# Performance work log

Hardware: AMD Instinct MI355X
Metric: run time of the kernel (lower is better)

## Reference

```python
import jax, jax.numpy as jnp
import numpy as np

N_NODES = 100000
N_EDGES = 1600000
D_IN = 128
D_HID = 128
LATENT = 64
N_GRAPHS = 512


def setup_inputs() -> dict:
    key = jax.random.key(0)
    ks = jax.random.split(key, 10)
    x = jax.random.normal(ks[0], (N_NODES, D_IN), dtype=jnp.float32)
    edge_index = jax.random.randint(ks[1], (2, N_EDGES), 0, N_NODES, dtype=jnp.int64)
    batch = jnp.sort(jax.random.randint(ks[2], (N_NODES,), 0, N_GRAPHS, dtype=jnp.int64))
    def lin(k, fan_in, fan_out):
        return jax.random.normal(k, (fan_in, fan_out), dtype=jnp.float32) / np.sqrt(fan_in)
    W1 = lin(ks[3], D_IN, D_HID); b1 = jnp.zeros((D_HID,), jnp.float32)
    W2 = lin(ks[4], D_HID, D_HID); b2 = jnp.zeros((D_HID,), jnp.float32)
    W3 = lin(ks[5], D_HID, 2 * LATENT); b3 = jnp.zeros((2 * LATENT,), jnp.float32)
    return {"x": x, "edge_index": edge_index, "batch": batch,
            "W1": W1, "b1": b1, "W2": W2, "b2": b2, "W3": W3, "b3": b3}


def _gcn_norm(edge_index, n_nodes):
    # PyG GCNConv default: add self-loops, symmetric normalization
    loop = jnp.arange(n_nodes, dtype=edge_index.dtype)
    src = jnp.concatenate([edge_index[0], loop])
    dst = jnp.concatenate([edge_index[1], loop])
    deg = jax.ops.segment_sum(jnp.ones_like(dst, dtype=jnp.float32), dst,
                              num_segments=n_nodes)
    dinv = jnp.where(deg > 0, jax.lax.rsqrt(deg), 0.0)
    norm = dinv[src] * dinv[dst]  # [E + N]
    return src, dst, norm


def _gcn_conv(x, W, b, src, dst, norm, n_nodes):
    h = x @ W                               # [N, d_out]
    msg = h[src] * norm[:, None]            # gather + scale, [E+N, d_out]
    agg = jax.ops.segment_sum(msg, dst, num_segments=n_nodes)
    return agg + b


def reference(x, edge_index, batch, W1, b1, W2, b2, W3, b3):
    n = x.shape[0]
    src, dst, norm = _gcn_norm(edge_index, n)
    h = jax.nn.relu(_gcn_conv(x, W1, b1, src, dst, norm, n))
    h = jax.nn.relu(_gcn_conv(h, W2, b2, src, dst, norm, n))
    h = _gcn_conv(h, W3, b3, src, dst, norm, n)
    # scatter_mean over batch ids -> [num_graphs, 2*latent]
    cnt = jax.ops.segment_sum(jnp.ones((n,), jnp.float32), batch,
                              num_segments=N_GRAPHS)
    summed = jax.ops.segment_sum(h, batch, num_segments=N_GRAPHS)
    return summed / jnp.maximum(cnt, 1.0)[:, None]
```

## Files before the change

### kernel.cpp

```cpp
#include <hip/hip_runtime.h>
#include <stdint.h>

typedef unsigned short u16;
typedef unsigned int   u32;

#define N_NODES  100000
#define N_EDGES  1600000
#define DFEAT    128
#define N_GRAPHS 512

#define NBKT   391
#define NBLK_E 782
#define LBUF   8192

typedef float f32x4 __attribute__((ext_vector_type(4)));
typedef short s16x8 __attribute__((ext_vector_type(8)));

__device__ __forceinline__ float bflo(u32 u) { return __uint_as_float(u << 16); }
__device__ __forceinline__ float bfhi(u32 u) { return __uint_as_float(u & 0xffff0000u); }
__device__ __forceinline__ u16 f2bf(float f) {
  u32 u = __float_as_uint(f);
  return (u16)((u + 0x7fffu + ((u >> 16) & 1u)) >> 16);
}
__device__ __forceinline__ u32 pack2(float f0, float f1) {
  return (u32)f2bf(f0) | ((u32)f2bf(f1) << 16);
}

__global__ void detect_k(const int* __restrict__ ei, int* __restrict__ flag) {
  int t = threadIdx.x;
  int v = ei[2 * t + 1];
  unsigned long long m = __ballot(v != 0);
  if (t == 0) *flag = (m == 0ull) ? 1 : 0;
}

__device__ __forceinline__ int ld_src(const int* ei, int m, int e) {
  return m ? ei[2 * e] : ei[e];
}
__device__ __forceinline__ int ld_dst(const int* ei, int m, int e) {
  return m ? ei[2 * (N_EDGES + e)] : ei[N_EDGES + e];
}


__global__ __launch_bounds__(256) void histA_k(const int* __restrict__ ei,
                                               const int* __restrict__ flag,
                                               int* __restrict__ ghist) {
  __shared__ int hist[NBKT];
  int t = threadIdx.x, b = blockIdx.x;
  for (int i = t; i < NBKT; i += 256) hist[i] = 0;
  __syncthreads();
  int m = *flag;
  int e0 = b * 2048;
#pragma unroll
  for (int p = 0; p < 8; p++) {
    int e = e0 + p * 256 + t;
    if (e < N_EDGES) atomicAdd(&hist[ld_dst(ei, m, e) >> 8], 1);
  }
  __syncthreads();
  for (int i = t; i < NBKT; i += 256) ghist[b * NBKT + i] = hist[i];
}

__global__ __launch_bounds__(256) void scanB1_k(int* __restrict__ ghist,
                                                int* __restrict__ gtot) {
  __shared__ int a[1024];
  __shared__ int ts[256];
  int t = threadIdx.x, k = blockIdx.x;
  for (int i = t; i < 1024; i += 256) a[i] = (i < NBLK_E) ? ghist[i * NBKT + k] : 0;
  __syncthreads();
  int b4 = t * 4;
  int x0 = a[b4], x1 = a[b4 + 1], x2 = a[b4 + 2], x3 = a[b4 + 3];
  int tot = x0 + x1 + x2 + x3;
  ts[t] = tot;
  for (int off = 1; off < 256; off <<= 1) {
    __syncthreads(); int add = (t >= off) ? ts[t - off] : 0;
    __syncthreads(); ts[t] += add;
  }
  __syncthreads();
  int excl = ts[t] - tot;
  a[b4] = excl; a[b4 + 1] = excl + x0; a[b4 + 2] = excl + x0 + x1; a[b4 + 3] = excl + x0 + x1 + x2;
  __syncthreads();
  for (int i = t; i < NBLK_E; i += 256) ghist[i * NBKT + k] = a[i];
  if (t == 255) gtot[k] = ts[255];
}

__global__ __launch_bounds__(512) void scanB2_k(const int* __restrict__ gtot,
                                                int* __restrict__ bbase) {
  __shared__ int tmp[512];
  int t = threadIdx.x;
  int v = (t < NBKT) ? gtot[t] : 0;
  tmp[t] = v;
  for (int off = 1; off < 512; off <<= 1) {
    __syncthreads(); int add = (t >= off) ? tmp[t - off] : 0;
    __syncthreads(); tmp[t] += add;
  }
  __syncthreads();
  if (t < NBKT) bbase[t] = tmp[t] - v;
  if (t == 0) bbase[NBKT] = N_EDGES;
}

__global__ __launch_bounds__(256) void scatterC_k(const int* __restrict__ ei,
                                                  const int* __restrict__ flag,
                                                  const int* __restrict__ obase,
                                                  const int* __restrict__ bbase,
                                                  u32* __restrict__ colpk) {
  __shared__ int cur[NBKT];
  int t = threadIdx.x, b = blockIdx.x;
  for (int i = t; i < NBKT; i += 256) cur[i] = bbase[i] + obase[b * NBKT + i];
  __syncthreads();
  int m = *flag;
  int e0 = b * 2048;
#pragma unroll
  for (int p = 0; p < 8; p++) {
    int e = e0 + p * 256 + t;
    if (e < N_EDGES) {
      int d = ld_dst(ei, m, e);
      int s = ld_src(ei, m, e);
      int pos = atomicAdd(&cur[d >> 8], 1);
      colpk[pos] = (u32)s | ((u32)(d & 255) << 24);
    }
  }
}

__global__ __launch_bounds__(256) void fillD_k(const int* __restrict__ bbase,
                                               const u32* __restrict__ colpk,
                                               int* __restrict__ colarr,
                                               int* __restrict__ rowptr,
                                               float* __restrict__ dinv) {
  __shared__ int hist[256];
  __shared__ int cur[256];
  __shared__ int lbuf[LBUF];
  int t = threadIdx.x, b = blockIdx.x;
  int base = bbase[b], end = bbase[b + 1], cnt = end - base;
  hist[t] = 0;
  __syncthreads();
  for (int i = t; i < cnt; i += 256) atomicAdd(&hist[colpk[base + i] >> 24], 1);
  __syncthreads();
  int c = hist[t];
  cur[t] = c;
  for (int off = 1; off < 256; off <<= 1) {
    __syncthreads(); int add = (t >= off) ? cur[t - off] : 0;
    __syncthreads(); cur[t] += add;
  }
  __syncthreads();
  int excl = cur[t] - c;
  int node = b * 256 + t;
  if (node < N_NODES) {
    rowptr[node] = base + excl;
    dinv[node] = rsqrtf((float)(c + 1));
  }
  if (b == NBKT - 1 && t == 0) rowptr[N_NODES] = N_EDGES;
  __syncthreads();
  cur[t] = excl;
  __syncthreads();
  for (int i = t; i < cnt; i += 256) {
    u32 v = colpk[base + i];
    int slot = atomicAdd(&cur[v >> 24], 1);
    if (slot < LBUF) lbuf[slot] = (int)(v & 0x00FFFFFFu);
  }
  __syncthreads();
  for (int i = t; i < cnt; i += 256) colarr[base + i] = lbuf[i];
}

__global__ void cvt_x_k(const float* __restrict__ X, u32* __restrict__ XB) {
  int i = blockIdx.x * 256 + threadIdx.x;
  float2 v = ((const float2*)X)[i];
  XB[i] = pack2(v.x, v.y);
}

__global__ void cvt_w_k(const float* __restrict__ W1, const float* __restrict__ W2,
                        const float* __restrict__ W3, u16* __restrict__ T1,
                        u16* __restrict__ T2, u16* __restrict__ T3) {
  const float* W = (blockIdx.x == 0) ? W1 : (blockIdx.x == 1) ? W2 : W3;
  u16* T         = (blockIdx.x == 0) ? T1 : (blockIdx.x == 1) ? T2 : T3;
  for (int i = threadIdx.x; i < DFEAT * DFEAT; i += 256) {
    int n = i >> 7, k = i & 127;
    T[i] = f2bf(W[k * DFEAT + n]);
  }
}

#define LP 136

__global__ __launch_bounds__(256, 1) void gemm_scale_k(const u16* __restrict__ X,
                                                       const u16* __restrict__ Wt,
                                                       const float* __restrict__ dinv,
                                                       u16* __restrict__ Y, int nrows) {
  __shared__ u16 sX[64 * LP];
  __shared__ u16 sW[128 * LP];
  int tid = threadIdx.x;
  int r0 = blockIdx.x * 64;

  for (int c = tid; c < 2048; c += 256) {
    int row = c >> 4, off = (c & 15) * 8;
    *(uint4*)(&sW[row * LP + off]) = *(const uint4*)(Wt + row * DFEAT + off);
  }
  for (int c = tid; c < 1024; c += 256) {
    int row = c >> 4, off = (c & 15) * 8;
    int grow = r0 + row;
    uint4 v;
    if (grow < nrows) v = *(const uint4*)(X + (size_t)grow * DFEAT + off);
    else              v = make_uint4(0, 0, 0, 0);
    *(uint4*)(&sX[row * LP + off]) = v;
  }
  __syncthreads();

  int wave = tid >> 6, lane = tid & 63;
  int q = lane >> 4, r = lane & 15;
  int wr0 = wave * 16;

  f32x4 acc[8];
#pragma unroll
  for (int i = 0; i < 8; i++) acc[i] = (f32x4){0.f, 0.f, 0.f, 0.f};

#pragma unroll
  for (int kk = 0; kk < 4; kk++) {
    int k0 = kk * 32;
    s16x8 a = *(const s16x8*)(&sX[(wr0 + r) * LP + k0 + q * 8]);
#pragma unroll
    for (int nt = 0; nt < 8; nt++) {
      s16x8 b = *(const s16x8*)(&sW[(nt * 16 + r) * LP + k0 + q * 8]);
      acc[nt] = __builtin_amdgcn_mfma_f32_16x16x32_bf16(a, b, acc[nt], 0, 0, 0);
    }
  }

#pragma unroll
  for (int i = 0; i < 4; i++) {
    int grow = r0 + wr0 + q * 4 + i;
    if (grow < nrows) {
      float dv = dinv[grow];
#pragma unroll
      for (int nt = 0; nt < 8; nt++) {
        Y[(size_t)grow * DFEAT + nt * 16 + r] = f2bf(acc[nt][i] * dv);
      }
    }
  }
}

struct Acc8 {
  float a0, a1, a2, a3, a4, a5, a6, a7;
  __device__ __forceinline__ void add(uint4 v) {
    a0 += bflo(v.x); a1 += bfhi(v.x); a2 += bflo(v.y); a3 += bfhi(v.y);
    a4 += bflo(v.z); a5 += bfhi(v.z); a6 += bflo(v.w); a7 += bfhi(v.w);
  }
};

__global__ __launch_bounds__(256) void agg_k(const u32* __restrict__ HS,
                                             const float* __restrict__ dinv,
                                             const int* __restrict__ rowptr,
                                             const int* __restrict__ colidx,
                                             const float* __restrict__ bias,
                                             u32* __restrict__ OUT, int do_relu) {
  int t = threadIdx.x;
  int node = blockIdx.x * 16 + (t >> 4);
  int fp = t & 15;

  int s = rowptr[node], e = rowptr[node + 1];

  Acc8 A;
  uint4 v = *(const uint4*)(HS + (size_t)node * 64 + fp * 4);
  A.a0 = bflo(v.x); A.a1 = bfhi(v.x); A.a2 = bflo(v.y); A.a3 = bfhi(v.y);
  A.a4 = bflo(v.z); A.a5 = bfhi(v.z); A.a6 = bflo(v.w); A.a7 = bfhi(v.w);

  int j = s;
  for (; j + 4 <= e; j += 4) {
    int i0 = colidx[j], i1 = colidx[j + 1], i2 = colidx[j + 2], i3 = colidx[j + 3];
    uint4 w0 = *(const uint4*)(HS + (size_t)i0 * 64 + fp * 4);
    uint4 w1 = *(const uint4*)(HS + (size_t)i1 * 64 + fp * 4);
    uint4 w2 = *(const uint4*)(HS + (size_t)i2 * 64 + fp * 4);
    uint4 w3 = *(const uint4*)(HS + (size_t)i3 * 64 + fp * 4);
    A.add(w0); A.add(w1); A.add(w2); A.add(w3);
  }
  for (; j < e; j++) {
    int i0 = colidx[j];
    uint4 w0 = *(const uint4*)(HS + (size_t)i0 * 64 + fp * 4);
    A.add(w0);
  }

  float dv = dinv[node];
  float4 b0 = *(const float4*)(bias + fp * 8);
  float4 b1 = *(const float4*)(bias + fp * 8 + 4);
  float r0 = A.a0 * dv + b0.x, r1 = A.a1 * dv + b0.y;
  float r2 = A.a2 * dv + b0.z, r3 = A.a3 * dv + b0.w;
  float r4 = A.a4 * dv + b1.x, r5 = A.a5 * dv + b1.y;
  float r6 = A.a6 * dv + b1.z, r7 = A.a7 * dv + b1.w;
  if (do_relu) {
    r0 = fmaxf(r0, 0.f); r1 = fmaxf(r1, 0.f); r2 = fmaxf(r2, 0.f); r3 = fmaxf(r3, 0.f);
    r4 = fmaxf(r4, 0.f); r5 = fmaxf(r5, 0.f); r6 = fmaxf(r6, 0.f); r7 = fmaxf(r7, 0.f);
  }
  uint4 o;
  o.x = pack2(r0, r1); o.y = pack2(r2, r3); o.z = pack2(r4, r5); o.w = pack2(r6, r7);
  *(uint4*)(OUT + (size_t)node * 64 + fp * 4) = o;
}

__device__ __forceinline__ int lower_bound_i(const int* a, int n, int key, int shift) {
  int lo = 0, hi = n;
  while (lo < hi) {
    int mid = (lo + hi) >> 1;
    if (a[mid << shift] < key) lo = mid + 1; else hi = mid;
  }
  return lo;
}

__global__ __launch_bounds__(256) void pool_k(const u32* __restrict__ H,
                                              const int* __restrict__ batch,
                                              const int* __restrict__ flag,
                                              float* __restrict__ OUT) {
  int g = blockIdx.x;
  int m = *flag;
  int lo = lower_bound_i(batch, N_NODES, g, m);
  int hi = lower_bound_i(batch, N_NODES, g + 1, m);
  int cnt = hi - lo;
  int d2 = threadIdx.x & 63;
  int half = threadIdx.x >> 6;
  float a0 = 0.f, a1 = 0.f;
  for (int row = lo + half; row < hi; row += 4) {
    u32 v = H[(size_t)row * 64 + d2];
    a0 += bflo(v); a1 += bfhi(v);
  }
  __shared__ float red0[256], red1[256];
  red0[threadIdx.x] = a0; red1[threadIdx.x] = a1;
  __syncthreads();
  if (threadIdx.x < 64) {
    float s0 = red0[d2] + red0[d2 + 64] + red0[d2 + 128] + red0[d2 + 192];
    float s1 = red1[d2] + red1[d2 + 64] + red1[d2 + 128] + red1[d2 + 192];
    float inv = 1.0f / fmaxf((float)cnt, 1.0f);
    OUT[g * DFEAT + 2 * d2]     = s0 * inv;
    OUT[g * DFEAT + 2 * d2 + 1] = s1 * inv;
  }
}


extern "C" void kernel_launch(void* const* d_in, const int* in_sizes, int n_in,
                              void* d_out, int out_size, void* d_ws, size_t ws_size,
                              hipStream_t stream) {
  const float* x   = (const float*)d_in[0];
  const int* ei    = (const int*)d_in[1];
  const int* batch = (const int*)d_in[2];
  const float* W1  = (const float*)d_in[3];
  const float* b1  = (const float*)d_in[4];
  const float* W2  = (const float*)d_in[5];
  const float* b2  = (const float*)d_in[6];
  const float* W3  = (const float*)d_in[7];
  const float* b3  = (const float*)d_in[8];
  float* out = (float*)d_out;

  char* p = (char*)d_ws;
  size_t off = 0;
  auto carve = [&](size_t bytes) -> void* {
    void* q = p + off;
    off = (off + bytes + 255) & ~(size_t)255;
    return q;
  };
  int*   flag   = (int*)carve(256);
  int*   ghist  = (int*)carve((size_t)NBLK_E * NBKT * 4);
  int*   gtot   = (int*)carve(NBKT * 4);
  int*   bbase  = (int*)carve((NBKT + 1) * 4);
  int*   rowptr = (int*)carve((N_NODES + 1) * 4);
  float* dinv   = (float*)carve(N_NODES * 4);
  u32*   colpk  = (u32*)carve((size_t)N_EDGES * 4);
  int*   colarr = (int*)carve((size_t)N_EDGES * 4);
  u16*   Wt1    = (u16*)carve(DFEAT * DFEAT * 2);
  u16*   Wt2    = (u16*)carve(DFEAT * DFEAT * 2);
  u16*   Wt3    = (u16*)carve(DFEAT * DFEAT * 2);
  u32*   xb     = (u32*)carve((size_t)N_NODES * 64 * 4);
  u32*   bufA   = (u32*)carve((size_t)N_NODES * 64 * 4);
  u32*   bufB   = (u32*)carve((size_t)N_NODES * 64 * 4);
  (void)ws_size;

  detect_k<<<1, 64, 0, stream>>>(ei, flag);
  histA_k<<<NBLK_E, 256, 0, stream>>>(ei, flag, ghist);
  scanB1_k<<<NBKT, 256, 0, stream>>>(ghist, gtot);
  scanB2_k<<<1, 512, 0, stream>>>(gtot, bbase);
  scatterC_k<<<NBLK_E, 256, 0, stream>>>(ei, flag, ghist, bbase, colpk);
  fillD_k<<<NBKT, 256, 0, stream>>>(bbase, colpk, colarr, rowptr, dinv);

  cvt_x_k<<<25000, 256, 0, stream>>>(x, xb);
  cvt_w_k<<<3, 256, 0, stream>>>(W1, W2, W3, Wt1, Wt2, Wt3);

  const int GB = (N_NODES + 63) / 64;
  const int AB = N_NODES / 16;

  gemm_scale_k<<<GB, 256, 0, stream>>>((const u16*)xb, Wt1, dinv, (u16*)bufA, N_NODES);
  agg_k<<<AB, 256, 0, stream>>>(bufA, dinv, rowptr, colarr, b1, bufB, 1);
  gemm_scale_k<<<GB, 256, 0, stream>>>((const u16*)bufB, Wt2, dinv, (u16*)bufA, N_NODES);
  agg_k<<<AB, 256, 0, stream>>>(bufA, dinv, rowptr, colarr, b2, bufB, 1);
  gemm_scale_k<<<GB, 256, 0, stream>>>((const u16*)bufB, Wt3, dinv, (u16*)bufA, N_NODES);
  agg_k<<<AB, 256, 0, stream>>>(bufA, dinv, rowptr, colarr, b3, bufB, 0);
  pool_k<<<N_GRAPHS, 256, 0, stream>>>(bufB, batch, flag, out);
}
```

Baseline: 424.6 us.

## Fuse fp32->bf16 input conversion into GEMM, enlarge GEMM tile, cooperative colidx loads

Folds the separate x-to-bf16 conversion kernel into the first GEMM, which now reads fp32 directly and converts while staging into LDS. This removes one full pass over the input and its intermediate buffer. The edge-index detection and weight transpose are merged into a single prep kernel to save a launch. The GEMM tile grows to 128 rows per block with two M-subtiles per wave, reusing each B fragment across two MFMAs. The aggregation loop now loads 16 column indices cooperatively and broadcasts them with shuffles, unrolled by 8, to cut redundant index loads and raise memory-level parallelism.

```diff
diff --git a/kernel.cpp b/kernel.cpp
--- a/kernel.cpp
+++ b/kernel.cpp
@@ -26,18 +26,32 @@
   return (u32)f2bf(f0) | ((u32)f2bf(f1) << 16);
 }
 
-__global__ void detect_k(const int* __restrict__ ei, int* __restrict__ flag) {
-  int t = threadIdx.x;
-  int v = ei[2 * t + 1];
-  unsigned long long m = __ballot(v != 0);
-  if (t == 0) *flag = (m == 0ull) ? 1 : 0;
-}
-
 __device__ __forceinline__ int ld_src(const int* ei, int m, int e) {
   return m ? ei[2 * e] : ei[e];
 }
 __device__ __forceinline__ int ld_dst(const int* ei, int m, int e) {
   return m ? ei[2 * (N_EDGES + e)] : ei[N_EDGES + e];
+}
+
+__global__ __launch_bounds__(256) void prep_k(const int* __restrict__ ei, int* __restrict__ flag,
+                                              const float* __restrict__ W1, const float* __restrict__ W2,
+                                              const float* __restrict__ W3, u16* __restrict__ T1,
+                                              u16* __restrict__ T2, u16* __restrict__ T3) {
+  int t = threadIdx.x;
+  if (blockIdx.x == 0) {
+    if (t < 64) {
+      int v = ei[2 * t + 1];
+      unsigned long long m = __ballot(v != 0);
+      if (t == 0) *flag = (m == 0ull) ? 1 : 0;
+    }
+    return;
+  }
+  const float* W = (blockIdx.x == 1) ? W1 : (blockIdx.x == 2) ? W2 : W3;
+  u16* T         = (blockIdx.x == 1) ? T1 : (blockIdx.x == 2) ? T2 : T3;
+  for (int i = t; i < DFEAT * DFEAT; i += 256) {
+    int n = i >> 7, k = i & 127;
+    T[i] = f2bf(W[k * DFEAT + n]);
+  }
 }
 
 
@@ -160,75 +174,83 @@
   for (int i = t; i < cnt; i += 256) colarr[base + i] = lbuf[i];
 }
 
-__global__ void cvt_x_k(const float* __restrict__ X, u32* __restrict__ XB) {
-  int i = blockIdx.x * 256 + threadIdx.x;
-  float2 v = ((const float2*)X)[i];
-  XB[i] = pack2(v.x, v.y);
-}
-
-__global__ void cvt_w_k(const float* __restrict__ W1, const float* __restrict__ W2,
-                        const float* __restrict__ W3, u16* __restrict__ T1,
-                        u16* __restrict__ T2, u16* __restrict__ T3) {
-  const float* W = (blockIdx.x == 0) ? W1 : (blockIdx.x == 1) ? W2 : W3;
-  u16* T         = (blockIdx.x == 0) ? T1 : (blockIdx.x == 1) ? T2 : T3;
-  for (int i = threadIdx.x; i < DFEAT * DFEAT; i += 256) {
-    int n = i >> 7, k = i & 127;
-    T[i] = f2bf(W[k * DFEAT + n]);
-  }
-}
-
 #define LP 136
 
-__global__ __launch_bounds__(256, 1) void gemm_scale_k(const u16* __restrict__ X,
+__global__ __launch_bounds__(256, 1) void gemm_scale_k(const void* __restrict__ Xv,
+                                                       int x_is_f32,
                                                        const u16* __restrict__ Wt,
                                                        const float* __restrict__ dinv,
                                                        u16* __restrict__ Y, int nrows) {
-  __shared__ u16 sX[64 * LP];
+  __shared__ u16 sX[128 * LP];
   __shared__ u16 sW[128 * LP];
   int tid = threadIdx.x;
-  int r0 = blockIdx.x * 64;
+  int r0 = blockIdx.x * 128;
 
   for (int c = tid; c < 2048; c += 256) {
     int row = c >> 4, off = (c & 15) * 8;
     *(uint4*)(&sW[row * LP + off]) = *(const uint4*)(Wt + row * DFEAT + off);
   }
-  for (int c = tid; c < 1024; c += 256) {
-    int row = c >> 4, off = (c & 15) * 8;
-    int grow = r0 + row;
-    uint4 v;
-    if (grow < nrows) v = *(const uint4*)(X + (size_t)grow * DFEAT + off);
-    else              v = make_uint4(0, 0, 0, 0);
-    *(uint4*)(&sX[row * LP + off]) = v;
+  if (x_is_f32) {
+    const float* Xf = (const float*)Xv;
+    for (int c = tid; c < 2048; c += 256) {
+      int row = c >> 4, off = (c & 15) * 8;
+      int grow = r0 + row;
+      uint4 o = make_uint4(0, 0, 0, 0);
+      if (grow < nrows) {
+        const float* px = Xf + (size_t)grow * DFEAT + off;
+        float4 v0 = *(const float4*)px;
+        float4 v1 = *(const float4*)(px + 4);
+        o.x = pack2(v0.x, v0.y); o.y = pack2(v0.z, v0.w);
+        o.z = pack2(v1.x, v1.y); o.w = pack2(v1.z, v1.w);
+      }
+      *(uint4*)(&sX[row * LP + off]) = o;
+    }
+  } else {
+    const u16* Xb = (const u16*)Xv;
+    for (int c = tid; c < 2048; c += 256) {
+      int row = c >> 4, off = (c & 15) * 8;
+      int grow = r0 + row;
+      uint4 v = make_uint4(0, 0, 0, 0);
+      if (grow < nrows) v = *(const uint4*)(Xb + (size_t)grow * DFEAT + off);
+      *(uint4*)(&sX[row * LP + off]) = v;
+    }
   }
   __syncthreads();
 
   int wave = tid >> 6, lane = tid & 63;
   int q = lane >> 4, r = lane & 15;
-  int wr0 = wave * 16;
-
-  f32x4 acc[8];
-#pragma unroll
-  for (int i = 0; i < 8; i++) acc[i] = (f32x4){0.f, 0.f, 0.f, 0.f};
+  int wr0 = wave * 32;
+
+  f32x4 acc[2][8];
+#pragma unroll
+  for (int m = 0; m < 2; m++)
+#pragma unroll
+    for (int i = 0; i < 8; i++) acc[m][i] = (f32x4){0.f, 0.f, 0.f, 0.f};
 
 #pragma unroll
   for (int kk = 0; kk < 4; kk++) {
     int k0 = kk * 32;
-    s16x8 a = *(const s16x8*)(&sX[(wr0 + r) * LP + k0 + q * 8]);
+    s16x8 a0 = *(const s16x8*)(&sX[(wr0 + r) * LP + k0 + q * 8]);
+    s16x8 a1 = *(const s16x8*)(&sX[(wr0 + 16 + r) * LP + k0 + q * 8]);
 #pragma unroll
     for (int nt = 0; nt < 8; nt++) {
       s16x8 b = *(const s16x8*)(&sW[(nt * 16 + r) * LP + k0 + q * 8]);
-      acc[nt] = __builtin_amdgcn_mfma_f32_16x16x32_bf16(a, b, acc[nt], 0, 0, 0);
-    }
-  }
-
-#pragma unroll
-  for (int i = 0; i < 4; i++) {
-    int grow = r0 + wr0 + q * 4 + i;
-    if (grow < nrows) {
-      float dv = dinv[grow];
-#pragma unroll
-      for (int nt = 0; nt < 8; nt++) {
-        Y[(size_t)grow * DFEAT + nt * 16 + r] = f2bf(acc[nt][i] * dv);
+      acc[0][nt] = __builtin_amdgcn_mfma_f32_16x16x32_bf16(a0, b, acc[0][nt], 0, 0, 0);
+      acc[1][nt] = __builtin_amdgcn_mfma_f32_16x16x32_bf16(a1, b, acc[1][nt], 0, 0, 0);
+    }
+  }
+
+#pragma unroll
+  for (int m = 0; m < 2; m++) {
+#pragma unroll
+    for (int i = 0; i < 4; i++) {
+      int grow = r0 + wr0 + m * 16 + q * 4 + i;
+      if (grow < nrows) {
+        float dv = dinv[grow];
+#pragma unroll
+        for (int nt = 0; nt < 8; nt++) {
+          Y[(size_t)grow * DFEAT + nt * 16 + r] = f2bf(acc[m][nt][i] * dv);
+        }
       }
     }
   }
@@ -259,19 +281,40 @@
   A.a0 = bflo(v.x); A.a1 = bfhi(v.x); A.a2 = bflo(v.y); A.a3 = bfhi(v.y);
   A.a4 = bflo(v.z); A.a5 = bfhi(v.z); A.a6 = bflo(v.w); A.a7 = bfhi(v.w);
 
-  int j = s;
-  for (; j + 4 <= e; j += 4) {
-    int i0 = colidx[j], i1 = colidx[j + 1], i2 = colidx[j + 2], i3 = colidx[j + 3];
-    uint4 w0 = *(const uint4*)(HS + (size_t)i0 * 64 + fp * 4);
-    uint4 w1 = *(const uint4*)(HS + (size_t)i1 * 64 + fp * 4);
-    uint4 w2 = *(const uint4*)(HS + (size_t)i2 * 64 + fp * 4);
-    uint4 w3 = *(const uint4*)(HS + (size_t)i3 * 64 + fp * 4);
-    A.add(w0); A.add(w1); A.add(w2); A.add(w3);
-  }
-  for (; j < e; j++) {
-    int i0 = colidx[j];
-    uint4 w0 = *(const uint4*)(HS + (size_t)i0 * 64 + fp * 4);
-    A.add(w0);
+  for (int w = s; w < e; w += 16) {
+    int c = (w + fp < e) ? colidx[w + fp] : 0;
+    int n = min(16, e - w);
+    int j = 0;
+    for (; j + 8 <= n; j += 8) {
+      int i0 = __shfl(c, j, 16),     i1 = __shfl(c, j + 1, 16);
+      int i2 = __shfl(c, j + 2, 16), i3 = __shfl(c, j + 3, 16);
+      int i4 = __shfl(c, j + 4, 16), i5 = __shfl(c, j + 5, 16);
+      int i6 = __shfl(c, j + 6, 16), i7 = __shfl(c, j + 7, 16);
+      uint4 w0 = *(const uint4*)(HS + (size_t)i0 * 64 + fp * 4);
+      uint4 w1 = *(const uint4*)(HS + (size_t)i1 * 64 + fp * 4);
+      uint4 w2 = *(const uint4*)(HS + (size_t)i2 * 64 + fp * 4);
+      uint4 w3 = *(const uint4*)(HS + (size_t)i3 * 64 + fp * 4);
+      uint4 w4 = *(const uint4*)(HS + (size_t)i4 * 64 + fp * 4);
+      uint4 w5 = *(const uint4*)(HS + (size_t)i5 * 64 + fp * 4);
+      uint4 w6 = *(const uint4*)(HS + (size_t)i6 * 64 + fp * 4);
+      uint4 w7 = *(const uint4*)(HS + (size_t)i7 * 64 + fp * 4);
+      A.add(w0); A.add(w1); A.add(w2); A.add(w3);
+      A.add(w4); A.add(w5); A.add(w6); A.add(w7);
+    }
+    for (; j + 4 <= n; j += 4) {
+      int i0 = __shfl(c, j, 16),     i1 = __shfl(c, j + 1, 16);
+      int i2 = __shfl(c, j + 2, 16), i3 = __shfl(c, j + 3, 16);
+      uint4 w0 = *(const uint4*)(HS + (size_t)i0 * 64 + fp * 4);
+      uint4 w1 = *(const uint4*)(HS + (size_t)i1 * 64 + fp * 4);
+      uint4 w2 = *(const uint4*)(HS + (size_t)i2 * 64 + fp * 4);
+      uint4 w3 = *(const uint4*)(HS + (size_t)i3 * 64 + fp * 4);
+      A.add(w0); A.add(w1); A.add(w2); A.add(w3);
+    }
+    for (; j < n; j++) {
+      int i0 = __shfl(c, j, 16);
+      uint4 w0 = *(const uint4*)(HS + (size_t)i0 * 64 + fp * 4);
+      A.add(w0);
+    }
   }
 
   float dv = dinv[node];
@@ -360,29 +403,25 @@
   u16*   Wt1    = (u16*)carve(DFEAT * DFEAT * 2);
   u16*   Wt2    = (u16*)carve(DFEAT * DFEAT * 2);
   u16*   Wt3    = (u16*)carve(DFEAT * DFEAT * 2);
-  u32*   xb     = (u32*)carve((size_t)N_NODES * 64 * 4);
   u32*   bufA   = (u32*)carve((size_t)N_NODES * 64 * 4);
   u32*   bufB   = (u32*)carve((size_t)N_NODES * 64 * 4);
   (void)ws_size;
 
-  detect_k<<<1, 64, 0, stream>>>(ei, flag);
+  prep_k<<<4, 256, 0, stream>>>(ei, flag, W1, W2, W3, Wt1, Wt2, Wt3);
   histA_k<<<NBLK_E, 256, 0, stream>>>(ei, flag, ghist);
   scanB1_k<<<NBKT, 256, 0, stream>>>(ghist, gtot);
   scanB2_k<<<1, 512, 0, stream>>>(gtot, bbase);
   scatterC_k<<<NBLK_E, 256, 0, stream>>>(ei, flag, ghist, bbase, colpk);
   fillD_k<<<NBKT, 256, 0, stream>>>(bbase, colpk, colarr, rowptr, dinv);
 
-  cvt_x_k<<<25000, 256, 0, stream>>>(x, xb);
-  cvt_w_k<<<3, 256, 0, stream>>>(W1, W2, W3, Wt1, Wt2, Wt3);
-
-  const int GB = (N_NODES + 63) / 64;
+  const int GB = (N_NODES + 127) / 128;
   const int AB = N_NODES / 16;
 
-  gemm_scale_k<<<GB, 256, 0, stream>>>((const u16*)xb, Wt1, dinv, (u16*)bufA, N_NODES);
+  gemm_scale_k<<<GB, 256, 0, stream>>>((const void*)x, 1, Wt1, dinv, (u16*)bufA, N_NODES);
   agg_k<<<AB, 256, 0, stream>>>(bufA, dinv, rowptr, colarr, b1, bufB, 1);
-  gemm_scale_k<<<GB, 256, 0, stream>>>((const u16*)bufB, Wt2, dinv, (u16*)bufA, N_NODES);
+  gemm_scale_k<<<GB, 256, 0, stream>>>((const void*)bufB, 0, Wt2, dinv, (u16*)bufA, N_NODES);
   agg_k<<<AB, 256, 0, stream>>>(bufA, dinv, rowptr, colarr, b2, bufB, 1);
-  gemm_scale_k<<<GB, 256, 0, stream>>>((const u16*)bufB, Wt3, dinv, (u16*)bufA, N_NODES);
+  gemm_scale_k<<<GB, 256, 0, stream>>>((const void*)bufB, 0, Wt3, dinv, (u16*)bufA, N_NODES);
   agg_k<<<AB, 256, 0, stream>>>(bufA, dinv, rowptr, colarr, b3, bufB, 0);
   pool_k<<<N_GRAPHS, 256, 0, stream>>>(bufB, batch, flag, out);
 }
```

Result: faster. 412.9 us (-2.7%).
